# Kernel tuning notes

Hardware: AMD Instinct MI355X
Metric: run time of the kernel (lower is better)

## Reference

```python
import jax, jax.numpy as jnp
import numpy as np

N_HEADS = 16
K_SIZE = 4          # canon conv kernel size
GATE_BIAS = 2.0     # gate_bias_init
GATE_REG = 0.01     # gate_regularization_strength (type='l1')


def setup_inputs() -> dict:
    key = jax.random.key(0)
    ks = jax.random.split(key, 11)
    B, T, C, M = 2, 2048, 1024, 256
    rn = lambda k, shape, s=1.0: jax.random.normal(k, shape, dtype=jnp.float32) * s
    return {
        "x": rn(ks[0], (B, T, C)),
        "forward_memory": rn(ks[1], (B, M, C)),
        "reverse_memory": rn(ks[2], (B, M, C)),
        "w_q": rn(ks[3], (C, C), 0.02),
        "w_k": rn(ks[4], (C, C), 0.02),
        "w_v": rn(ks[5], (C, C), 0.02),
        "w_o": rn(ks[6], (C, C), 0.02),
        "gate_w": rn(ks[7], (C, N_HEADS), 0.02),
        "gate_b": jnp.full((N_HEADS,), GATE_BIAS, dtype=jnp.float32),
        "conv_w": rn(ks[8], (K_SIZE, 1, C), 0.05),  # depthwise, WIO layout
        "conv_b": rn(ks[9], (C,), 0.02),
    }


def reference(x, forward_memory, reverse_memory, w_q, w_k, w_v, w_o,
              gate_w, gate_b, conv_w, conv_b):
    B, T, C = x.shape
    h = N_HEADS
    d = C // h
    # projections; memory K/V use the same k/v projections and concat on seq dim
    q = x @ w_q                                                   # [B,T,C]
    k = jnp.concatenate([x @ w_k, forward_memory @ w_k, reverse_memory @ w_k], axis=1)
    v = jnp.concatenate([x @ w_v, forward_memory @ w_v, reverse_memory @ w_v], axis=1)
    S = k.shape[1]
    qh = q.reshape(B, T, h, d).transpose(0, 2, 1, 3)              # [B,h,T,d]
    kh = k.reshape(B, S, h, d).transpose(0, 2, 1, 3)              # [B,h,S,d]
    vh = v.reshape(B, S, h, d).transpose(0, 2, 1, 3)              # [B,h,S,d]
    scale = 1.0 / np.sqrt(d).astype(np.float32)
    scores = jnp.einsum('bhtd,bhsd->bhts', qh, kh) * scale        # [B,h,T,S]
    # causal mask on the chunk columns only; memory columns always visible
    causal = jnp.triu(jnp.ones((T, T), dtype=bool), 1)
    mask = jnp.concatenate([causal, jnp.zeros((T, S - T), dtype=bool)], axis=1)
    scores = jnp.where(mask[None, None], -jnp.inf, scores)
    w = jax.nn.softmax(scores, axis=-1)
    # split chunk vs memory attention and apply per-head sigmoid gate
    y_chunk = jnp.einsum('bhts,bhsd->bhtd', w[..., :T], vh[:, :, :T])
    y_mem = jnp.einsum('bhts,bhsd->bhtd', w[..., T:], vh[:, :, T:])
    g = jax.nn.sigmoid(q @ gate_w + gate_b)                       # [B,T,h]
    g = g.transpose(0, 2, 1)[..., None]                           # [B,h,T,1]
    y = y_chunk + g * y_mem
    gate_reg_loss = GATE_REG * jnp.mean(jnp.abs(g))
    attn = y.transpose(0, 2, 1, 3).reshape(B, T, C)
    # CanonConv: causal depthwise conv1d with residual
    xp = jnp.pad(attn, ((0, 0), (K_SIZE - 1, 0), (0, 0)))
    conv = jax.lax.conv_general_dilated(
        xp, conv_w, window_strides=(1,), padding='VALID',
        dimension_numbers=('NWC', 'WIO', 'NWC'), feature_group_count=C) + conv_b
    attn = attn + conv
    out = attn @ w_o
    return out, gate_reg_loss
```

## Files before the change

### kernel.cpp

```cpp
#include <hip/hip_runtime.h>
#include <hip/hip_bf16.h>

typedef __attribute__((ext_vector_type(8))) short short8;
typedef __attribute__((ext_vector_type(4))) short short4v;
typedef __attribute__((ext_vector_type(4))) float float4v;

#define B_ 2
#define T_ 2048
#define C_ 1024
#define H_ 16
#define D_ 64
#define M_ 256
#define S_ 2560

static __device__ __forceinline__ float bf2f(short s) {
    union { unsigned int u; float f; } v;
    v.u = ((unsigned int)(unsigned short)s) << 16;
    return v.f;
}
static __device__ __forceinline__ short f2bf(float f) {
    __hip_bfloat16 h = __float2bfloat16(f);
    return *reinterpret_cast<short*>(&h);
}
static __device__ __forceinline__ void gload_lds16(const short* g, short* l) {
    __builtin_amdgcn_global_load_lds(
        (const __attribute__((address_space(1))) void*)g,
        (__attribute__((address_space(3))) void*)l, 16, 0, 0);
}

__global__ __launch_bounds__(256) void cvt_bf16(const float* __restrict__ src,
                                                short* __restrict__ dst, int n8) {
    int i = blockIdx.x * 256 + threadIdx.x;
    if (i >= n8) return;
    float4v a = *(const float4v*)(src + (size_t)i * 8);
    float4v b = *(const float4v*)(src + (size_t)i * 8 + 4);
    short8 o;
    o[0] = f2bf(a[0]); o[1] = f2bf(a[1]); o[2] = f2bf(a[2]); o[3] = f2bf(a[3]);
    o[4] = f2bf(b[0]); o[5] = f2bf(b[1]); o[6] = f2bf(b[2]); o[7] = f2bf(b[3]);
    *(short8*)(dst + (size_t)i * 8) = o;
}

__global__ void transpose_k(const float* __restrict__ W, short* __restrict__ Wt) {
    __shared__ float tile[32][33];
    int tx = threadIdx.x, ty = threadIdx.y;
    int bx = blockIdx.x * 32, by = blockIdx.y * 32;
    tile[ty][tx] = W[(size_t)(by + ty) * 1024 + bx + tx];
    __syncthreads();
    Wt[(size_t)(bx + ty) * 1024 + by + tx] = f2bf(tile[tx][ty]);
}

__global__ __launch_bounds__(256) void gwt_cvt(const float* __restrict__ gw,
                                               short* __restrict__ gwt) {
    int idx = blockIdx.x * 256 + threadIdx.x;
    int h = idx >> 10, k = idx & 1023;
    gwt[idx] = f2bf(8.0f * gw[k * 16 + h]);
}

static __device__ __forceinline__ const short* concat_row(
    const short* x, const short* f, const short* rm, int r) {
    int b = (r >= S_) ? 1 : 0;
    int s = r - b * S_;
    if (s < T_)       return x  + ((size_t)b * T_ + s) * 1024;
    if (s < T_ + M_)  return f  + ((size_t)b * M_ + (s - T_)) * 1024;
    return rm + ((size_t)b * M_ + (s - T_ - M_)) * 1024;
}

__global__ __launch_bounds__(256) void qkv_fused(
    const short* __restrict__ x_bf, const short* __restrict__ fm_bf,
    const short* __restrict__ rm_bf, const short* __restrict__ wq_t,
    const short* __restrict__ wk_t, const short* __restrict__ wv_t,
    short* __restrict__ qb, short* __restrict__ kall,
    short* __restrict__ vallT) {
    __shared__ __align__(16) short As[128 * 32];
    __shared__ __align__(16) short Bs[128 * 32];
    const int tid = threadIdx.x;
    const int bid = blockIdx.x;
    int which, bm, bn;
    if (bid < 256)      { which = 0; bm = bid >> 3; bn = bid & 7; }
    else if (bid < 576) { which = 1; int t = bid - 256; bm = t >> 3; bn = t & 7; }
    else                { which = 2; int t = bid - 576; bm = t >> 3; bn = t & 7; }
    const short* Bt = (which == 0) ? wq_t : (which == 1) ? wk_t : wv_t;

    const int lane = tid & 63, w = tid >> 6;
    const int l15 = lane & 15, quad = lane >> 4;
    const int wm = (w >> 1) * 64, wn = (w & 1) * 64;
    const int sub = lane >> 2, u = lane & 3;

    const short* a0p;
    const short* a1p;
    {
        int r0 = bm * 128 + w * 32 + sub;
        if (which == 0) {
            a0p = x_bf + (size_t)r0 * 1024 + u * 8;
            a1p = x_bf + (size_t)(r0 + 16) * 1024 + u * 8;
        } else {
            a0p = concat_row(x_bf, fm_bf, rm_bf, r0) + u * 8;
            a1p = concat_row(x_bf, fm_bf, rm_bf, r0 + 16) + u * 8;
        }
    }
    const short* b0p = Bt + (size_t)(bn * 128 + w * 32 + sub) * 1024 + u * 8;
    const short* b1p = b0p + (size_t)16 * 1024;
    short* Asw = As + w * 1024;
    short* Bsw = Bs + w * 1024;

    float4v acc[4][4];
    const float4v zero = {0.f, 0.f, 0.f, 0.f};
#pragma unroll
    for (int i = 0; i < 4; ++i)
#pragma unroll
        for (int j = 0; j < 4; ++j) acc[i][j] = zero;

    for (int k0 = 0; k0 < 1024; k0 += 32) {
        __syncthreads();
        gload_lds16(a0p + k0, Asw);
        gload_lds16(a1p + k0, Asw + 512);
        gload_lds16(b0p + k0, Bsw);
        gload_lds16(b1p + k0, Bsw + 512);
        __syncthreads();
        short8 af[4], bfr[4];
#pragma unroll
        for (int i = 0; i < 4; ++i)
            af[i] = *(const short8*)(&As[(wm + i * 16 + l15) * 32 + quad * 8]);
#pragma unroll
        for (int j = 0; j < 4; ++j)
            bfr[j] = *(const short8*)(&Bs[(wn + j * 16 + l15) * 32 + quad * 8]);
#pragma unroll
        for (int i = 0; i < 4; ++i)
#pragma unroll
            for (int j = 0; j < 4; ++j)
                acc[i][j] = __builtin_amdgcn_mfma_f32_16x16x32_bf16(af[i], bfr[j], acc[i][j], 0, 0, 0);
    }

    const int mbase = bm * 128 + wm, nbase = bn * 128 + wn;
    if (which == 2) {
#pragma unroll
        for (int i = 0; i < 4; ++i)
#pragma unroll
            for (int j = 0; j < 4; ++j) {
                int sbase = mbase + i * 16 + quad * 4;
                int ng = nbase + j * 16 + l15;
                int b = (sbase >= S_) ? 1 : 0, s = sbase - b * S_;
                int hh = ng >> 6, d = ng & 63;
                short4v pk;
#pragma unroll
                for (int r = 0; r < 4; ++r) pk[r] = f2bf(acc[i][j][r]);
                *(short4v*)(vallT + ((size_t)((b * 16 + hh) * 64 + d)) * S_ + s) = pk;
            }
    } else {
        short* Co = (which == 0) ? qb : kall;
        const float scale = (which == 0) ? 0.125f : 1.0f;
#pragma unroll
        for (int i = 0; i < 4; ++i)
#pragma unroll
            for (int j = 0; j < 4; ++j)
#pragma unroll
                for (int r = 0; r < 4; ++r) {
                    int mg = mbase + i * 16 + quad * 4 + r;
                    int ng = nbase + j * 16 + l15;
                    Co[(size_t)mg * 1024 + ng] = f2bf(acc[i][j][r] * scale);
                }
    }
}

__global__ __launch_bounds__(256) void gemm128_wo(
    const short* __restrict__ A0, const short* __restrict__ Bt,
    float* __restrict__ Co) {
    __shared__ __align__(16) short As[128 * 32];
    __shared__ __align__(16) short Bs[128 * 32];
    const int tid = threadIdx.x;
    const int bm = blockIdx.y, bn = blockIdx.x;
    const int lane = tid & 63, w = tid >> 6;
    const int l15 = lane & 15, quad = lane >> 4;
    const int wm = (w >> 1) * 64, wn = (w & 1) * 64;
    const int sub = lane >> 2, u = lane & 3;

    const short* a0p = A0 + (size_t)(bm * 128 + w * 32 + sub) * 1024 + u * 8;
    const short* a1p = a0p + (size_t)16 * 1024;
    const short* b0p = Bt + (size_t)(bn * 128 + w * 32 + sub) * 1024 + u * 8;
    const short* b1p = b0p + (size_t)16 * 1024;
    short* Asw = As + w * 1024;
    short* Bsw = Bs + w * 1024;

    float4v acc[4][4];
    const float4v zero = {0.f, 0.f, 0.f, 0.f};
#pragma unroll
    for (int i = 0; i < 4; ++i)
#pragma unroll
        for (int j = 0; j < 4; ++j) acc[i][j] = zero;

    for (int k0 = 0; k0 < 1024; k0 += 32) {
        __syncthreads();
        gload_lds16(a0p + k0, Asw);
        gload_lds16(a1p + k0, Asw + 512);
        gload_lds16(b0p + k0, Bsw);
        gload_lds16(b1p + k0, Bsw + 512);
        __syncthreads();
        short8 af[4], bfr[4];
#pragma unroll
        for (int i = 0; i < 4; ++i)
            af[i] = *(const short8*)(&As[(wm + i * 16 + l15) * 32 + quad * 8]);
#pragma unroll
        for (int j = 0; j < 4; ++j)
            bfr[j] = *(const short8*)(&Bs[(wn + j * 16 + l15) * 32 + quad * 8]);
#pragma unroll
        for (int i = 0; i < 4; ++i)
#pragma unroll
            for (int j = 0; j < 4; ++j)
                acc[i][j] = __builtin_amdgcn_mfma_f32_16x16x32_bf16(af[i], bfr[j], acc[i][j], 0, 0, 0);
    }

    const int mbase = bm * 128 + wm, nbase = bn * 128 + wn;
#pragma unroll
    for (int i = 0; i < 4; ++i)
#pragma unroll
        for (int j = 0; j < 4; ++j)
#pragma unroll
            for (int r = 0; r < 4; ++r)
                Co[(size_t)(mbase + i * 16 + quad * 4 + r) * 1024 + nbase + j * 16 + l15] = acc[i][j][r];
}

__global__ __launch_bounds__(256) void gate_kernel(
    const short* __restrict__ q, const short* __restrict__ gwt,
    const float* __restrict__ gate_b, float* __restrict__ gbuf,
    float* __restrict__ loss) {
    const int tid = threadIdx.x;
    const int lane = tid & 63, w = tid >> 6;
    const int l15 = lane & 15, quad = lane >> 4;
    const int row0 = blockIdx.x * 64 + w * 16;
    const size_t abase = (size_t)(row0 + l15) * 1024;
    const size_t bbase = (size_t)l15 * 1024;

    float4v acc = {0.f, 0.f, 0.f, 0.f};
#pragma unroll 4
    for (int k0 = 0; k0 < 1024; k0 += 32) {
        short8 af = *(const short8*)(q + abase + k0 + quad * 8);
        short8 bf = *(const short8*)(gwt + bbase + k0 + quad * 8);
        acc = __builtin_amdgcn_mfma_f32_16x16x32_bf16(af, bf, acc, 0, 0, 0);
    }
    const int head = l15;
    const int tbase = row0 + quad * 4;
    const int b = tbase >> 11, t = tbase & 2047;
    const float gbias = gate_b[head];
    float4v g;
    float lsum = 0.f;
#pragma unroll
    for (int r = 0; r < 4; ++r) {
        g[r] = 1.0f / (1.0f + __expf(-(acc[r] + gbias)));
        lsum += g[r];
    }
    *(float4v*)(gbuf + ((size_t)(b * 16 + head)) * 2048 + t) = g;
    lsum += __shfl_xor(lsum, 1);  lsum += __shfl_xor(lsum, 2);
    lsum += __shfl_xor(lsum, 4);  lsum += __shfl_xor(lsum, 8);
    lsum += __shfl_xor(lsum, 16); lsum += __shfl_xor(lsum, 32);
    if (lane == 0) atomicAdd(loss, lsum);
}

__global__ __launch_bounds__(256, 3) void attn_kernel(
    const short* __restrict__ q, const short* __restrict__ kall,
    const short* __restrict__ vallT, const float* __restrict__ gbuf,
    short* __restrict__ attn) {
    __shared__ __align__(16) short Kt[64 * 68];
    __shared__ __align__(16) short Vs[64 * 68];
    __shared__ __align__(16) short Pt[4 * 16 * 72];
    const int tid = threadIdx.x;
    const int bid = blockIdx.x;
    const int qt = 31 - (bid >> 5);
    const int bh = bid & 31, b = bh >> 4, h = bh & 15;
    const int q0 = qt * 64;
    const int lane = tid & 63, w = tid >> 6;
    const int l15 = lane & 15, quad = lane >> 4;
    const int srow = tid >> 2, scol = (tid & 3) * 16;

    const int trow = q0 + w * 16 + l15;
    short8 qf[2];
    qf[0] = *(const short8*)(q + ((size_t)(b * T_ + trow)) * 1024 + h * 64 + quad * 8);
    qf[1] = *(const short8*)(q + ((size_t)(b * T_ + trow)) * 1024 + h * 64 + 32 + quad * 8);

    const float4v zero = {0.f, 0.f, 0.f, 0.f};
    float4v acc_c[4], acc_m[4];
#pragma unroll
    for (int n = 0; n < 4; ++n) { acc_c[n] = zero; acc_m[n] = zero; }
    float lsum = 0.0f;

    short* Pw = &Pt[w * 16 * 72];
    const int ntiles = qt + 9;

    const size_t kbase = (size_t)b * S_ * 1024 + h * 64;
    const size_t vbase = (size_t)bh * 64 * S_;

    short8 pk0, pk1, pv0, pv1;
    {
        pk0 = *(const short8*)(kall + kbase + (size_t)srow * 1024 + scol);
        pk1 = *(const short8*)(kall + kbase + (size_t)srow * 1024 + scol + 8);
        pv0 = *(const short8*)(vallT + vbase + (size_t)srow * S_ + scol);
        pv1 = *(const short8*)(vallT + vbase + (size_t)srow * S_ + scol + 8);
    }

    for (int t = 0; t < ntiles; ++t) {
        __syncthreads();
        *(short8*)(&Kt[srow * 68 + scol])     = pk0;
        *(short8*)(&Kt[srow * 68 + scol + 8]) = pk1;
        *(short8*)(&Vs[srow * 68 + scol])     = pv0;
        *(short8*)(&Vs[srow * 68 + scol + 8]) = pv1;
        __syncthreads();
        if (t + 1 < ntiles) {
            const int t1 = t + 1;
            const int s1 = (t1 <= qt) ? t1 * 64 : T_ + (t1 - qt - 1) * 64;
            pk0 = *(const short8*)(kall + kbase + (size_t)(s1 + srow) * 1024 + scol);
            pk1 = *(const short8*)(kall + kbase + (size_t)(s1 + srow) * 1024 + scol + 8);
            pv0 = *(const short8*)(vallT + vbase + (size_t)srow * S_ + s1 + scol);
            pv1 = *(const short8*)(vallT + vbase + (size_t)srow * S_ + s1 + scol + 8);
        }

        float4v c[4];
#pragma unroll
        for (int n = 0; n < 4; ++n) c[n] = zero;
#pragma unroll
        for (int ks = 0; ks < 2; ++ks) {
            short8 kb[4];
#pragma unroll
            for (int n = 0; n < 4; ++n)
                kb[n] = *(const short8*)(&Kt[(n * 16 + l15) * 68 + ks * 32 + quad * 8]);
#pragma unroll
            for (int n = 0; n < 4; ++n)
                c[n] = __builtin_amdgcn_mfma_f32_16x16x32_bf16(kb[n], qf[ks], c[n], 0, 0, 0);
        }

        const bool diag = (t == qt);
#pragma unroll
        for (int n = 0; n < 4; ++n) {
            float p[4];
#pragma unroll
            for (int r = 0; r < 4; ++r) {
                p[r] = __expf(c[n][r] - 8.0f);
                if (diag && (n * 16 + quad * 4 + r > w * 16 + l15)) p[r] = 0.0f;
                lsum += p[r];
            }
            short4v pk4;
#pragma unroll
            for (int r = 0; r < 4; ++r) pk4[r] = f2bf(p[r]);
            *(short4v*)(&Pw[l15 * 72 + n * 16 + quad * 4]) = pk4;
        }

        float4v* accp = (t > qt) ? acc_m : acc_c;
#pragma unroll
        for (int ks = 0; ks < 2; ++ks) {
            short8 pb = *(const short8*)(&Pw[l15 * 72 + ks * 32 + quad * 8]);
#pragma unroll
            for (int m = 0; m < 4; ++m) {
                short8 vb = *(const short8*)(&Vs[(m * 16 + l15) * 68 + ks * 32 + quad * 8]);
                accp[m] = __builtin_amdgcn_mfma_f32_16x16x32_bf16(vb, pb, accp[m], 0, 0, 0);
            }
        }
    }

    lsum += __shfl_xor(lsum, 16);
    lsum += __shfl_xor(lsum, 32);
    const float g = gbuf[((size_t)b * 16 + h) * 2048 + q0 + w * 16 + l15];
    const float inv = 1.0f / lsum;

    __syncthreads();
    short* Dt = Kt;
#pragma unroll
    for (int m = 0; m < 4; ++m) {
        short4v o4;
#pragma unroll
        for (int r = 0; r < 4; ++r)
            o4[r] = f2bf((acc_c[m][r] + g * acc_m[m][r]) * inv);
        *(short4v*)(&Dt[(w * 16 + l15) * 68 + m * 16 + quad * 4]) = o4;
    }
    __syncthreads();
    short8 o0 = *(const short8*)(&Dt[srow * 68 + scol]);
    short8 o1 = *(const short8*)(&Dt[srow * 68 + scol + 8]);
    *(short8*)(attn + ((size_t)(b * T_ + q0 + srow)) * 1024 + h * 64 + scol) = o0;
    *(short8*)(attn + ((size_t)(b * T_ + q0 + srow)) * 1024 + h * 64 + scol + 8) = o1;
}

__global__ __launch_bounds__(256) void conv_kernel(
    const short* __restrict__ attn, const float* __restrict__ conv_w,
    const float* __restrict__ conv_b, short* __restrict__ attn2) {
    const int idx = blockIdx.x * 256 + threadIdx.x;
    const int c8 = (idx & 127) * 8;
    const int bt = idx >> 7;
    const int t = bt & 2047;
    float acc[8];
    short8 base = *(const short8*)(attn + (size_t)bt * 1024 + c8);
#pragma unroll
    for (int jj = 0; jj < 8; ++jj) acc[jj] = bf2f(base[jj]) + conv_b[c8 + jj];
#pragma unroll
    for (int j = 0; j < 4; ++j) {
        int ts = t - 3 + j;
        if (ts >= 0) {
            short8 xv = *(const short8*)(attn + (size_t)(bt - 3 + j) * 1024 + c8);
#pragma unroll
            for (int jj = 0; jj < 8; ++jj)
                acc[jj] += bf2f(xv[jj]) * conv_w[j * 1024 + c8 + jj];
        }
    }
    short8 outv;
#pragma unroll
    for (int jj = 0; jj < 8; ++jj) outv[jj] = f2bf(acc[jj]);
    *(short8*)(attn2 + (size_t)bt * 1024 + c8) = outv;
}

__global__ void loss_fin(const float* __restrict__ loss, float* __restrict__ out) {
    out[0] = 0.01f * loss[0] / 65536.0f;
}

extern "C" void kernel_launch(void* const* d_in, const int* in_sizes, int n_in,
                              void* d_out, int out_size, void* d_ws, size_t ws_size,
                              hipStream_t stream) {
    const float* x  = (const float*)d_in[0];
    const float* fm = (const float*)d_in[1];
    const float* rm = (const float*)d_in[2];
    const float* wq = (const float*)d_in[3];
    const float* wk = (const float*)d_in[4];
    const float* wv = (const float*)d_in[5];
    const float* wo = (const float*)d_in[6];
    const float* gw = (const float*)d_in[7];
    const float* gb = (const float*)d_in[8];
    const float* cw = (const float*)d_in[9];
    const float* cb = (const float*)d_in[10];
    float* out = (float*)d_out;

    char* ws = (char*)d_ws;
    const size_t MB = 1u << 20;
    short* wq_t  = (short*)(ws + 0 * MB);
    short* wk_t  = (short*)(ws + 2 * MB);
    short* wv_t  = (short*)(ws + 4 * MB);
    short* wo_t  = (short*)(ws + 6 * MB);
    short* x_bf  = (short*)(ws + 8 * MB);
    short* fm_bf = (short*)(ws + 16 * MB);
    short* rm_bf = (short*)(ws + 17 * MB);
    short* qb    = (short*)(ws + 18 * MB);
    short* kall  = (short*)(ws + 26 * MB);
    short* vallT = (short*)(ws + 36 * MB);
    float* gbuf  = (float*)(ws + 46 * MB);
    float* lossp = (float*)(ws + 46 * MB + 256 * 1024);
    short* attnb = x_bf;
    short* attn2 = qb;
    short* gwt   = fm_bf;

    cvt_bf16<<<2048, 256, 0, stream>>>(x, x_bf, 524288);
    cvt_bf16<<<256, 256, 0, stream>>>(fm, fm_bf, 65536);
    cvt_bf16<<<256, 256, 0, stream>>>(rm, rm_bf, 65536);

    dim3 tb(32, 32);
    transpose_k<<<dim3(32, 32), tb, 0, stream>>>(wq, wq_t);
    transpose_k<<<dim3(32, 32), tb, 0, stream>>>(wk, wk_t);
    transpose_k<<<dim3(32, 32), tb, 0, stream>>>(wv, wv_t);
    transpose_k<<<dim3(32, 32), tb, 0, stream>>>(wo, wo_t);

    qkv_fused<<<896, 256, 0, stream>>>(x_bf, fm_bf, rm_bf, wq_t, wk_t, wv_t,
                                       qb, kall, vallT);

    hipMemsetAsync(lossp, 0, 4, stream);
    gwt_cvt<<<64, 256, 0, stream>>>(gw, gwt);
    gate_kernel<<<64, 256, 0, stream>>>(qb, gwt, gb, gbuf, lossp);
    attn_kernel<<<1024, 256, 0, stream>>>(qb, kall, vallT, gbuf, attnb);
    conv_kernel<<<2048, 256, 0, stream>>>(attnb, cw, cb, attn2);
    gemm128_wo<<<dim3(8, 32), 256, 0, stream>>>(attn2, wo_t, out);
    loss_fin<<<1, 1, 0, stream>>>(lossp, out + (size_t)4096 * 1024);
}
```

Measured before the change: 272.0 us.

## Fuse prep kernels, fold gate projection into QKV, enlarge attention tiles, retile Wo GEMM

Merges all bf16 conversions, weight transposes and the gate-weight prep into one launch. The gate weight is precomputed as Wq·gate_w, so the gate GEMM runs on x inside the QKV kernel as extra blocks, and the loss finalisation moves into the conv kernel. Attention now processes 128 query rows per block with two query groups per wave, which halves K/V tile loads per query but lowers occupancy. The Wo GEMM uses 64x128 tiles to launch more blocks. Together these cut launch count and memory traffic, at the cost of more register pressure and a gate precomputation that runs in fp32 on the device.

```diff
diff --git a/kernel.cpp b/kernel.cpp
--- a/kernel.cpp
+++ b/kernel.cpp
@@ -28,32 +28,53 @@
         (__attribute__((address_space(3))) void*)l, 16, 0, 0);
 }
 
-__global__ __launch_bounds__(256) void cvt_bf16(const float* __restrict__ src,
-                                                short* __restrict__ dst, int n8) {
-    int i = blockIdx.x * 256 + threadIdx.x;
-    if (i >= n8) return;
-    float4v a = *(const float4v*)(src + (size_t)i * 8);
-    float4v b = *(const float4v*)(src + (size_t)i * 8 + 4);
-    short8 o;
-    o[0] = f2bf(a[0]); o[1] = f2bf(a[1]); o[2] = f2bf(a[2]); o[3] = f2bf(a[3]);
-    o[4] = f2bf(b[0]); o[5] = f2bf(b[1]); o[6] = f2bf(b[2]); o[7] = f2bf(b[3]);
-    *(short8*)(dst + (size_t)i * 8) = o;
-}
-
-__global__ void transpose_k(const float* __restrict__ W, short* __restrict__ Wt) {
+__global__ __launch_bounds__(256) void prep_kernel(
+    const float* __restrict__ x, const float* __restrict__ fm,
+    const float* __restrict__ rm, const float* __restrict__ wq,
+    const float* __restrict__ wk, const float* __restrict__ wv,
+    const float* __restrict__ wo, const float* __restrict__ gw,
+    short* __restrict__ x_bf, short* __restrict__ fm_bf,
+    short* __restrict__ rm_bf, short* __restrict__ wq_t,
+    short* __restrict__ wk_t, short* __restrict__ wv_t,
+    short* __restrict__ wo_t, short* __restrict__ wg2t,
+    float* __restrict__ lossp) {
     __shared__ float tile[32][33];
-    int tx = threadIdx.x, ty = threadIdx.y;
-    int bx = blockIdx.x * 32, by = blockIdx.y * 32;
-    tile[ty][tx] = W[(size_t)(by + ty) * 1024 + bx + tx];
-    __syncthreads();
-    Wt[(size_t)(bx + ty) * 1024 + by + tx] = f2bf(tile[tx][ty]);
-}
-
-__global__ __launch_bounds__(256) void gwt_cvt(const float* __restrict__ gw,
-                                               short* __restrict__ gwt) {
-    int idx = blockIdx.x * 256 + threadIdx.x;
-    int h = idx >> 10, k = idx & 1023;
-    gwt[idx] = f2bf(8.0f * gw[k * 16 + h]);
+    const int bid = blockIdx.x, tid = threadIdx.x;
+    if (bid < 2560) {
+        const float* src; short* dst; int i;
+        if (bid < 2048)      { src = x;  dst = x_bf;  i = bid * 256 + tid; }
+        else if (bid < 2304) { src = fm; dst = fm_bf; i = (bid - 2048) * 256 + tid; }
+        else                 { src = rm; dst = rm_bf; i = (bid - 2304) * 256 + tid; }
+        float4v a = *(const float4v*)(src + (size_t)i * 8);
+        float4v b = *(const float4v*)(src + (size_t)i * 8 + 4);
+        short8 o;
+        o[0] = f2bf(a[0]); o[1] = f2bf(a[1]); o[2] = f2bf(a[2]); o[3] = f2bf(a[3]);
+        o[4] = f2bf(b[0]); o[5] = f2bf(b[1]); o[6] = f2bf(b[2]); o[7] = f2bf(b[3]);
+        *(short8*)(dst + (size_t)i * 8) = o;
+    } else if (bid < 6656) {
+        const int g = bid - 2560;
+        const int m = g >> 10, tI = g & 1023;
+        const float* W = (m == 0) ? wq : (m == 1) ? wk : (m == 2) ? wv : wo;
+        short* Wt      = (m == 0) ? wq_t : (m == 1) ? wk_t : (m == 2) ? wv_t : wo_t;
+        const int ty = tid >> 5, tx = tid & 31;
+        const int bx = (tI & 31) << 5, by = (tI >> 5) << 5;
+#pragma unroll
+        for (int r = 0; r < 4; ++r)
+            tile[ty + r * 8][tx] = W[(size_t)(by + ty + r * 8) * 1024 + bx + tx];
+        __syncthreads();
+#pragma unroll
+        for (int r = 0; r < 4; ++r)
+            Wt[(size_t)(bx + ty + r * 8) * 1024 + by + tx] = f2bf(tile[tx][ty + r * 8]);
+    } else {
+        if (bid == 6656 && tid == 0) *lossp = 0.0f;
+        const int idx = (bid - 6656) * 256 + tid;
+        const int k = idx >> 4, hh = idx & 15;
+        float acc = 0.0f;
+#pragma unroll 4
+        for (int c = 0; c < 1024; ++c)
+            acc += wq[(size_t)k * 1024 + c] * gw[c * 16 + hh];
+        wg2t[hh * 1024 + k] = f2bf(acc);
+    }
 }
 
 static __device__ __forceinline__ const short* concat_row(
@@ -69,20 +90,54 @@
     const short* __restrict__ x_bf, const short* __restrict__ fm_bf,
     const short* __restrict__ rm_bf, const short* __restrict__ wq_t,
     const short* __restrict__ wk_t, const short* __restrict__ wv_t,
+    const short* __restrict__ wg2t, const float* __restrict__ gate_b,
     short* __restrict__ qb, short* __restrict__ kall,
-    short* __restrict__ vallT) {
+    short* __restrict__ vallT, float* __restrict__ gbuf,
+    float* __restrict__ loss) {
     __shared__ __align__(16) short As[128 * 32];
     __shared__ __align__(16) short Bs[128 * 32];
     const int tid = threadIdx.x;
     const int bid = blockIdx.x;
+    const int lane = tid & 63, w = tid >> 6;
+    const int l15 = lane & 15, quad = lane >> 4;
+
+    if (bid >= 896) {
+        const int gblk = bid - 896;
+        const int row0 = gblk * 64 + w * 16;
+        const size_t abase = (size_t)(row0 + l15) * 1024;
+        const size_t bbase = (size_t)l15 * 1024;
+        float4v acc = {0.f, 0.f, 0.f, 0.f};
+#pragma unroll 4
+        for (int k0 = 0; k0 < 1024; k0 += 32) {
+            short8 af = *(const short8*)(x_bf + abase + k0 + quad * 8);
+            short8 bf = *(const short8*)(wg2t + bbase + k0 + quad * 8);
+            acc = __builtin_amdgcn_mfma_f32_16x16x32_bf16(af, bf, acc, 0, 0, 0);
+        }
+        const int head = l15;
+        const int tbase = row0 + quad * 4;
+        const int b = tbase >> 11, t = tbase & 2047;
+        const float gbias = gate_b[head];
+        float4v g;
+        float lsum = 0.f;
+#pragma unroll
+        for (int r = 0; r < 4; ++r) {
+            g[r] = 1.0f / (1.0f + __expf(-(acc[r] + gbias)));
+            lsum += g[r];
+        }
+        *(float4v*)(gbuf + ((size_t)(b * 16 + head)) * 2048 + t) = g;
+        lsum += __shfl_xor(lsum, 1);  lsum += __shfl_xor(lsum, 2);
+        lsum += __shfl_xor(lsum, 4);  lsum += __shfl_xor(lsum, 8);
+        lsum += __shfl_xor(lsum, 16); lsum += __shfl_xor(lsum, 32);
+        if (lane == 0) atomicAdd(loss, lsum);
+        return;
+    }
+
     int which, bm, bn;
     if (bid < 256)      { which = 0; bm = bid >> 3; bn = bid & 7; }
     else if (bid < 576) { which = 1; int t = bid - 256; bm = t >> 3; bn = t & 7; }
     else                { which = 2; int t = bid - 576; bm = t >> 3; bn = t & 7; }
     const short* Bt = (which == 0) ? wq_t : (which == 1) ? wk_t : wv_t;
 
-    const int lane = tid & 63, w = tid >> 6;
-    const int l15 = lane & 15, quad = lane >> 4;
     const int wm = (w >> 1) * 64, wn = (w & 1) * 64;
     const int sub = lane >> 2, u = lane & 3;
 
@@ -162,249 +217,231 @@
     }
 }
 
-__global__ __launch_bounds__(256) void gemm128_wo(
+__global__ __launch_bounds__(256, 2) void attn_kernel(
+    const short* __restrict__ q, const short* __restrict__ kall,
+    const short* __restrict__ vallT, const float* __restrict__ gbuf,
+    short* __restrict__ attn) {
+    __shared__ __align__(16) short KV[128 * 68];
+    __shared__ __align__(16) short Pt[4 * 32 * 68];
+    const int tid = threadIdx.x;
+    const int bid = blockIdx.x;
+    const int qt = 15 - (bid >> 5);
+    const int bh = bid & 31, b = bh >> 4, h = bh & 15;
+    const int q0 = qt * 128;
+    const int lane = tid & 63, w = tid >> 6;
+    const int l15 = lane & 15, quad = lane >> 4;
+    const int srow = tid >> 2, scol = (tid & 3) * 16;
+    short* Kt = KV;
+    short* Vs = KV + 64 * 68;
+
+    short8 qf[2][2];
+#pragma unroll
+    for (int qg = 0; qg < 2; ++qg)
+#pragma unroll
+        for (int ks = 0; ks < 2; ++ks)
+            qf[qg][ks] = *(const short8*)(q + ((size_t)(b * T_ + q0 + w * 32 + qg * 16 + l15)) * 1024
+                                          + h * 64 + ks * 32 + quad * 8);
+
+    const float4v zero = {0.f, 0.f, 0.f, 0.f};
+    float4v accC[2][4], accM[2][4];
+#pragma unroll
+    for (int g = 0; g < 2; ++g)
+#pragma unroll
+        for (int m = 0; m < 4; ++m) { accC[g][m] = zero; accM[g][m] = zero; }
+    float lsum[2] = {0.0f, 0.0f};
+
+    short* Pw = &Pt[w * 32 * 68];
+    const int ntiles = 2 * qt + 10;
+
+    const size_t kbase = (size_t)b * S_ * 1024 + h * 64;
+    const size_t vbase = (size_t)bh * 64 * S_;
+
+    short8 pk0, pk1, pv0, pv1;
+    pk0 = *(const short8*)(kall + kbase + (size_t)srow * 1024 + scol);
+    pk1 = *(const short8*)(kall + kbase + (size_t)srow * 1024 + scol + 8);
+    pv0 = *(const short8*)(vallT + vbase + (size_t)srow * S_ + scol);
+    pv1 = *(const short8*)(vallT + vbase + (size_t)srow * S_ + scol + 8);
+
+    for (int t = 0; t < ntiles; ++t) {
+        __syncthreads();
+        *(short8*)(&Kt[srow * 68 + scol])     = pk0;
+        *(short8*)(&Kt[srow * 68 + scol + 8]) = pk1;
+        *(short8*)(&Vs[srow * 68 + scol])     = pv0;
+        *(short8*)(&Vs[srow * 68 + scol + 8]) = pv1;
+        __syncthreads();
+        if (t + 1 < ntiles) {
+            const int t1 = t + 1;
+            const int s1 = (t1 <= 2 * qt + 1) ? t1 * 64 : T_ + (t1 - 2 * qt - 2) * 64;
+            pk0 = *(const short8*)(kall + kbase + (size_t)(s1 + srow) * 1024 + scol);
+            pk1 = *(const short8*)(kall + kbase + (size_t)(s1 + srow) * 1024 + scol + 8);
+            pv0 = *(const short8*)(vallT + vbase + (size_t)srow * S_ + s1 + scol);
+            pv1 = *(const short8*)(vallT + vbase + (size_t)srow * S_ + s1 + scol + 8);
+        }
+
+        short8 kb[2][4], vb[2][4];
+#pragma unroll
+        for (int ks = 0; ks < 2; ++ks)
+#pragma unroll
+            for (int n = 0; n < 4; ++n) {
+                kb[ks][n] = *(const short8*)(&Kt[(n * 16 + l15) * 68 + ks * 32 + quad * 8]);
+                vb[ks][n] = *(const short8*)(&Vs[(n * 16 + l15) * 68 + ks * 32 + quad * 8]);
+            }
+
+        const bool last2 = (t >= 2 * qt) && (t <= 2 * qt + 1);
+        const bool mem = (t > 2 * qt + 1);
+        const int srel = (t - 2 * qt) * 64;
+
+#pragma unroll
+        for (int qg = 0; qg < 2; ++qg) {
+            const int qmin = w * 32 + qg * 16;
+            if (last2 && srel > qmin + 15) continue;
+
+            float4v c[4];
+#pragma unroll
+            for (int n = 0; n < 4; ++n) c[n] = zero;
+#pragma unroll
+            for (int ks = 0; ks < 2; ++ks)
+#pragma unroll
+                for (int n = 0; n < 4; ++n)
+                    c[n] = __builtin_amdgcn_mfma_f32_16x16x32_bf16(kb[ks][n], qf[qg][ks], c[n], 0, 0, 0);
+
+#pragma unroll
+            for (int n = 0; n < 4; ++n) {
+                float p[4];
+                short4v pk4;
+#pragma unroll
+                for (int r = 0; r < 4; ++r) {
+                    p[r] = __expf(c[n][r] - 8.0f);
+                    if (last2 && (srel + n * 16 + quad * 4 + r > qmin + l15)) p[r] = 0.0f;
+                    lsum[qg] += p[r];
+                    pk4[r] = f2bf(p[r]);
+                }
+                *(short4v*)(&Pw[(qg * 16 + l15) * 68 + n * 16 + quad * 4]) = pk4;
+            }
+
+            float4v* accp = mem ? accM[qg] : accC[qg];
+#pragma unroll
+            for (int ks = 0; ks < 2; ++ks) {
+                short8 pb = *(const short8*)(&Pw[(qg * 16 + l15) * 68 + ks * 32 + quad * 8]);
+#pragma unroll
+                for (int m = 0; m < 4; ++m)
+                    accp[m] = __builtin_amdgcn_mfma_f32_16x16x32_bf16(vb[ks][m], pb, accp[m], 0, 0, 0);
+            }
+        }
+    }
+
+    __syncthreads();
+    short* Dt = KV;
+#pragma unroll
+    for (int qg = 0; qg < 2; ++qg) {
+        float ls = lsum[qg];
+        ls += __shfl_xor(ls, 16);
+        ls += __shfl_xor(ls, 32);
+        const int ql = w * 32 + qg * 16 + l15;
+        const float g = gbuf[((size_t)b * 16 + h) * 2048 + q0 + ql];
+        const float inv = 1.0f / ls;
+#pragma unroll
+        for (int m = 0; m < 4; ++m) {
+            short4v o4;
+#pragma unroll
+            for (int r = 0; r < 4; ++r)
+                o4[r] = f2bf((accC[qg][m][r] + g * accM[qg][m][r]) * inv);
+            *(short4v*)(&Dt[ql * 68 + m * 16 + quad * 4]) = o4;
+        }
+    }
+    __syncthreads();
+    const int orow = tid >> 1, ocol = (tid & 1) * 32;
+    const size_t obase = ((size_t)(b * T_ + q0 + orow)) * 1024 + h * 64 + ocol;
+#pragma unroll
+    for (int u2 = 0; u2 < 4; ++u2) {
+        short8 ov = *(const short8*)(&Dt[orow * 68 + ocol + u2 * 8]);
+        *(short8*)(attn + obase + u2 * 8) = ov;
+    }
+}
+
+__global__ __launch_bounds__(256) void conv_kernel(
+    const short* __restrict__ attn, const float* __restrict__ conv_w,
+    const float* __restrict__ conv_b, short* __restrict__ attn2,
+    const float* __restrict__ lossp, float* __restrict__ out) {
+    const int idx = blockIdx.x * 256 + threadIdx.x;
+    if (idx == 0) out[(size_t)4096 * 1024] = 0.01f * lossp[0] / 65536.0f;
+    const int c8 = (idx & 127) * 8;
+    const int bt = idx >> 7;
+    const int t = bt & 2047;
+    float acc[8];
+    short8 base = *(const short8*)(attn + (size_t)bt * 1024 + c8);
+#pragma unroll
+    for (int jj = 0; jj < 8; ++jj) acc[jj] = bf2f(base[jj]) + conv_b[c8 + jj];
+#pragma unroll
+    for (int j = 0; j < 4; ++j) {
+        int ts = t - 3 + j;
+        if (ts >= 0) {
+            short8 xv = *(const short8*)(attn + (size_t)(bt - 3 + j) * 1024 + c8);
+#pragma unroll
+            for (int jj = 0; jj < 8; ++jj)
+                acc[jj] += bf2f(xv[jj]) * conv_w[j * 1024 + c8 + jj];
+        }
+    }
+    short8 outv;
+#pragma unroll
+    for (int jj = 0; jj < 8; ++jj) outv[jj] = f2bf(acc[jj]);
+    *(short8*)(attn2 + (size_t)bt * 1024 + c8) = outv;
+}
+
+__global__ __launch_bounds__(256) void wo_gemm(
     const short* __restrict__ A0, const short* __restrict__ Bt,
     float* __restrict__ Co) {
-    __shared__ __align__(16) short As[128 * 32];
+    __shared__ __align__(16) short As[64 * 32];
     __shared__ __align__(16) short Bs[128 * 32];
     const int tid = threadIdx.x;
     const int bm = blockIdx.y, bn = blockIdx.x;
     const int lane = tid & 63, w = tid >> 6;
     const int l15 = lane & 15, quad = lane >> 4;
-    const int wm = (w >> 1) * 64, wn = (w & 1) * 64;
-    const int sub = lane >> 2, u = lane & 3;
-
-    const short* a0p = A0 + (size_t)(bm * 128 + w * 32 + sub) * 1024 + u * 8;
-    const short* a1p = a0p + (size_t)16 * 1024;
-    const short* b0p = Bt + (size_t)(bn * 128 + w * 32 + sub) * 1024 + u * 8;
-    const short* b1p = b0p + (size_t)16 * 1024;
-    short* Asw = As + w * 1024;
-    short* Bsw = Bs + w * 1024;
-
-    float4v acc[4][4];
+    const int wm = (w >> 1) * 32, wn = (w & 1) * 64;
+    const int sr = lane >> 2, u = lane & 3;
+
+    const short* ap  = A0 + (size_t)(bm * 64 + w * 16 + sr) * 1024 + u * 8;
+    const short* b0p = Bt + (size_t)(bn * 128 + w * 16 + sr) * 1024 + u * 8;
+    const short* b1p = b0p + (size_t)64 * 1024;
+    short* Asw  = As + w * 512;
+    short* Bsw0 = Bs + w * 512;
+    short* Bsw1 = Bs + 2048 + w * 512;
+
+    float4v acc[2][4];
     const float4v zero = {0.f, 0.f, 0.f, 0.f};
 #pragma unroll
-    for (int i = 0; i < 4; ++i)
+    for (int i = 0; i < 2; ++i)
 #pragma unroll
         for (int j = 0; j < 4; ++j) acc[i][j] = zero;
 
     for (int k0 = 0; k0 < 1024; k0 += 32) {
         __syncthreads();
-        gload_lds16(a0p + k0, Asw);
-        gload_lds16(a1p + k0, Asw + 512);
-        gload_lds16(b0p + k0, Bsw);
-        gload_lds16(b1p + k0, Bsw + 512);
-        __syncthreads();
-        short8 af[4], bfr[4];
-#pragma unroll
-        for (int i = 0; i < 4; ++i)
+        gload_lds16(ap + k0, Asw);
+        gload_lds16(b0p + k0, Bsw0);
+        gload_lds16(b1p + k0, Bsw1);
+        __syncthreads();
+        short8 af[2], bfr[4];
+#pragma unroll
+        for (int i = 0; i < 2; ++i)
             af[i] = *(const short8*)(&As[(wm + i * 16 + l15) * 32 + quad * 8]);
 #pragma unroll
         for (int j = 0; j < 4; ++j)
             bfr[j] = *(const short8*)(&Bs[(wn + j * 16 + l15) * 32 + quad * 8]);
 #pragma unroll
-        for (int i = 0; i < 4; ++i)
+        for (int i = 0; i < 2; ++i)
 #pragma unroll
             for (int j = 0; j < 4; ++j)
                 acc[i][j] = __builtin_amdgcn_mfma_f32_16x16x32_bf16(af[i], bfr[j], acc[i][j], 0, 0, 0);
     }
 
-    const int mbase = bm * 128 + wm, nbase = bn * 128 + wn;
-#pragma unroll
-    for (int i = 0; i < 4; ++i)
+    const int mbase = bm * 64 + wm, nbase = bn * 128 + wn;
+#pragma unroll
+    for (int i = 0; i < 2; ++i)
 #pragma unroll
         for (int j = 0; j < 4; ++j)
 #pragma unroll
             for (int r = 0; r < 4; ++r)
                 Co[(size_t)(mbase + i * 16 + quad * 4 + r) * 1024 + nbase + j * 16 + l15] = acc[i][j][r];
-}
-
-__global__ __launch_bounds__(256) void gate_kernel(
-    const short* __restrict__ q, const short* __restrict__ gwt,
-    const float* __restrict__ gate_b, float* __restrict__ gbuf,
-    float* __restrict__ loss) {
-    const int tid = threadIdx.x;
-    const int lane = tid & 63, w = tid >> 6;
-    const int l15 = lane & 15, quad = lane >> 4;
-    const int row0 = blockIdx.x * 64 + w * 16;
-    const size_t abase = (size_t)(row0 + l15) * 1024;
-    const size_t bbase = (size_t)l15 * 1024;
-
-    float4v acc = {0.f, 0.f, 0.f, 0.f};
-#pragma unroll 4
-    for (int k0 = 0; k0 < 1024; k0 += 32) {
-        short8 af = *(const short8*)(q + abase + k0 + quad * 8);
-        short8 bf = *(const short8*)(gwt + bbase + k0 + quad * 8);
-        acc = __builtin_amdgcn_mfma_f32_16x16x32_bf16(af, bf, acc, 0, 0, 0);
-    }
-    const int head = l15;
-    const int tbase = row0 + quad * 4;
-    const int b = tbase >> 11, t = tbase & 2047;
-    const float gbias = gate_b[head];
-    float4v g;
-    float lsum = 0.f;
-#pragma unroll
-    for (int r = 0; r < 4; ++r) {
-        g[r] = 1.0f / (1.0f + __expf(-(acc[r] + gbias)));
-        lsum += g[r];
-    }
-    *(float4v*)(gbuf + ((size_t)(b * 16 + head)) * 2048 + t) = g;
-    lsum += __shfl_xor(lsum, 1);  lsum += __shfl_xor(lsum, 2);
-    lsum += __shfl_xor(lsum, 4);  lsum += __shfl_xor(lsum, 8);
-    lsum += __shfl_xor(lsum, 16); lsum += __shfl_xor(lsum, 32);
-    if (lane == 0) atomicAdd(loss, lsum);
-}
-
-__global__ __launch_bounds__(256, 3) void attn_kernel(
-    const short* __restrict__ q, const short* __restrict__ kall,
-    const short* __restrict__ vallT, const float* __restrict__ gbuf,
-    short* __restrict__ attn) {
-    __shared__ __align__(16) short Kt[64 * 68];
-    __shared__ __align__(16) short Vs[64 * 68];
-    __shared__ __align__(16) short Pt[4 * 16 * 72];
-    const int tid = threadIdx.x;
-    const int bid = blockIdx.x;
-    const int qt = 31 - (bid >> 5);
-    const int bh = bid & 31, b = bh >> 4, h = bh & 15;
-    const int q0 = qt * 64;
-    const int lane = tid & 63, w = tid >> 6;
-    const int l15 = lane & 15, quad = lane >> 4;
-    const int srow = tid >> 2, scol = (tid & 3) * 16;
-
-    const int trow = q0 + w * 16 + l15;
-    short8 qf[2];
-    qf[0] = *(const short8*)(q + ((size_t)(b * T_ + trow)) * 1024 + h * 64 + quad * 8);
-    qf[1] = *(const short8*)(q + ((size_t)(b * T_ + trow)) * 1024 + h * 64 + 32 + quad * 8);
-
-    const float4v zero = {0.f, 0.f, 0.f, 0.f};
-    float4v acc_c[4], acc_m[4];
-#pragma unroll
-    for (int n = 0; n < 4; ++n) { acc_c[n] = zero; acc_m[n] = zero; }
-    float lsum = 0.0f;
-
-    short* Pw = &Pt[w * 16 * 72];
-    const int ntiles = qt + 9;
-
-    const size_t kbase = (size_t)b * S_ * 1024 + h * 64;
-    const size_t vbase = (size_t)bh * 64 * S_;
-
-    short8 pk0, pk1, pv0, pv1;
-    {
-        pk0 = *(const short8*)(kall + kbase + (size_t)srow * 1024 + scol);
-        pk1 = *(const short8*)(kall + kbase + (size_t)srow * 1024 + scol + 8);
-        pv0 = *(const short8*)(vallT + vbase + (size_t)srow * S_ + scol);
-        pv1 = *(const short8*)(vallT + vbase + (size_t)srow * S_ + scol + 8);
-    }
-
-    for (int t = 0; t < ntiles; ++t) {
-        __syncthreads();
-        *(short8*)(&Kt[srow * 68 + scol])     = pk0;
-        *(short8*)(&Kt[srow * 68 + scol + 8]) = pk1;
-        *(short8*)(&Vs[srow * 68 + scol])     = pv0;
-        *(short8*)(&Vs[srow * 68 + scol + 8]) = pv1;
-        __syncthreads();
-        if (t + 1 < ntiles) {
-            const int t1 = t + 1;
-            const int s1 = (t1 <= qt) ? t1 * 64 : T_ + (t1 - qt - 1) * 64;
-            pk0 = *(const short8*)(kall + kbase + (size_t)(s1 + srow) * 1024 + scol);
-            pk1 = *(const short8*)(kall + kbase + (size_t)(s1 + srow) * 1024 + scol + 8);
-            pv0 = *(const short8*)(vallT + vbase + (size_t)srow * S_ + s1 + scol);
-            pv1 = *(const short8*)(vallT + vbase + (size_t)srow * S_ + s1 + scol + 8);
-        }
-
-        float4v c[4];
-#pragma unroll
-        for (int n = 0; n < 4; ++n) c[n] = zero;
-#pragma unroll
-        for (int ks = 0; ks < 2; ++ks) {
-            short8 kb[4];
-#pragma unroll
-            for (int n = 0; n < 4; ++n)
-                kb[n] = *(const short8*)(&Kt[(n * 16 + l15) * 68 + ks * 32 + quad * 8]);
-#pragma unroll
-            for (int n = 0; n < 4; ++n)
-                c[n] = __builtin_amdgcn_mfma_f32_16x16x32_bf16(kb[n], qf[ks], c[n], 0, 0, 0);
-        }
-
-        const bool diag = (t == qt);
-#pragma unroll
-        for (int n = 0; n < 4; ++n) {
-            float p[4];
-#pragma unroll
-            for (int r = 0; r < 4; ++r) {
-                p[r] = __expf(c[n][r] - 8.0f);
-                if (diag && (n * 16 + quad * 4 + r > w * 16 + l15)) p[r] = 0.0f;
-                lsum += p[r];
-            }
-            short4v pk4;
-#pragma unroll
-            for (int r = 0; r < 4; ++r) pk4[r] = f2bf(p[r]);
-            *(short4v*)(&Pw[l15 * 72 + n * 16 + quad * 4]) = pk4;
-        }
-
-        float4v* accp = (t > qt) ? acc_m : acc_c;
-#pragma unroll
-        for (int ks = 0; ks < 2; ++ks) {
-            short8 pb = *(const short8*)(&Pw[l15 * 72 + ks * 32 + quad * 8]);
-#pragma unroll
-            for (int m = 0; m < 4; ++m) {
-                short8 vb = *(const short8*)(&Vs[(m * 16 + l15) * 68 + ks * 32 + quad * 8]);
-                accp[m] = __builtin_amdgcn_mfma_f32_16x16x32_bf16(vb, pb, accp[m], 0, 0, 0);
-            }
-        }
-    }
-
-    lsum += __shfl_xor(lsum, 16);
-    lsum += __shfl_xor(lsum, 32);
-    const float g = gbuf[((size_t)b * 16 + h) * 2048 + q0 + w * 16 + l15];
-    const float inv = 1.0f / lsum;
-
-    __syncthreads();
-    short* Dt = Kt;
-#pragma unroll
-    for (int m = 0; m < 4; ++m) {
-        short4v o4;
-#pragma unroll
-        for (int r = 0; r < 4; ++r)
-            o4[r] = f2bf((acc_c[m][r] + g * acc_m[m][r]) * inv);
-        *(short4v*)(&Dt[(w * 16 + l15) * 68 + m * 16 + quad * 4]) = o4;
-    }
-    __syncthreads();
-    short8 o0 = *(const short8*)(&Dt[srow * 68 + scol]);
-    short8 o1 = *(const short8*)(&Dt[srow * 68 + scol + 8]);
-    *(short8*)(attn + ((size_t)(b * T_ + q0 + srow)) * 1024 + h * 64 + scol) = o0;
-    *(short8*)(attn + ((size_t)(b * T_ + q0 + srow)) * 1024 + h * 64 + scol + 8) = o1;
-}
-
-__global__ __launch_bounds__(256) void conv_kernel(
-    const short* __restrict__ attn, const float* __restrict__ conv_w,
-    const float* __restrict__ conv_b, short* __restrict__ attn2) {
-    const int idx = blockIdx.x * 256 + threadIdx.x;
-    const int c8 = (idx & 127) * 8;
-    const int bt = idx >> 7;
-    const int t = bt & 2047;
-    float acc[8];
-    short8 base = *(const short8*)(attn + (size_t)bt * 1024 + c8);
-#pragma unroll
-    for (int jj = 0; jj < 8; ++jj) acc[jj] = bf2f(base[jj]) + conv_b[c8 + jj];
-#pragma unroll
-    for (int j = 0; j < 4; ++j) {
-        int ts = t - 3 + j;
-        if (ts >= 0) {
-            short8 xv = *(const short8*)(attn + (size_t)(bt - 3 + j) * 1024 + c8);
-#pragma unroll
-            for (int jj = 0; jj < 8; ++jj)
-                acc[jj] += bf2f(xv[jj]) * conv_w[j * 1024 + c8 + jj];
-        }
-    }
-    short8 outv;
-#pragma unroll
-    for (int jj = 0; jj < 8; ++jj) outv[jj] = f2bf(acc[jj]);
-    *(short8*)(attn2 + (size_t)bt * 1024 + c8) = outv;
-}
-
-__global__ void loss_fin(const float* __restrict__ loss, float* __restrict__ out) {
-    out[0] = 0.01f * loss[0] / 65536.0f;
 }
 
 extern "C" void kernel_launch(void* const* d_in, const int* in_sizes, int n_in,
@@ -436,29 +473,17 @@
     short* kall  = (short*)(ws + 26 * MB);
     short* vallT = (short*)(ws + 36 * MB);
     float* gbuf  = (float*)(ws + 46 * MB);
-    float* lossp = (float*)(ws + 46 * MB + 256 * 1024);
+    float* lossp = (float*)(ws + 46 * MB + 262144);
+    short* wg2t  = (short*)(ws + 46 * MB + 262144 + 256);
     short* attnb = x_bf;
     short* attn2 = qb;
-    short* gwt   = fm_bf;
-
-    cvt_bf16<<<2048, 256, 0, stream>>>(x, x_bf, 524288);
-    cvt_bf16<<<256, 256, 0, stream>>>(fm, fm_bf, 65536);
-    cvt_bf16<<<256, 256, 0, stream>>>(rm, rm_bf, 65536);
-
-    dim3 tb(32, 32);
-    transpose_k<<<dim3(32, 32), tb, 0, stream>>>(wq, wq_t);
-    transpose_k<<<dim3(32, 32), tb, 0, stream>>>(wk, wk_t);
-    transpose_k<<<dim3(32, 32), tb, 0, stream>>>(wv, wv_t);
-    transpose_k<<<dim3(32, 32), tb, 0, stream>>>(wo, wo_t);
-
-    qkv_fused<<<896, 256, 0, stream>>>(x_bf, fm_bf, rm_bf, wq_t, wk_t, wv_t,
-                                       qb, kall, vallT);
-
-    hipMemsetAsync(lossp, 0, 4, stream);
-    gwt_cvt<<<64, 256, 0, stream>>>(gw, gwt);
-    gate_kernel<<<64, 256, 0, stream>>>(qb, gwt, gb, gbuf, lossp);
-    attn_kernel<<<1024, 256, 0, stream>>>(qb, kall, vallT, gbuf, attnb);
-    conv_kernel<<<2048, 256, 0, stream>>>(attnb, cw, cb, attn2);
-    gemm128_wo<<<dim3(8, 32), 256, 0, stream>>>(attn2, wo_t, out);
-    loss_fin<<<1, 1, 0, stream>>>(lossp, out + (size_t)4096 * 1024);
-}
+
+    prep_kernel<<<6720, 256, 0, stream>>>(x, fm, rm, wq, wk, wv, wo, gw,
+                                          x_bf, fm_bf, rm_bf, wq_t, wk_t, wv_t,
+                                          wo_t, wg2t, lossp);
+    qkv_fused<<<960, 256, 0, stream>>>(x_bf, fm_bf, rm_bf, wq_t, wk_t, wv_t,
+                                       wg2t, gb, qb, kall, vallT, gbuf, lossp);
+    attn_kernel<<<512, 256, 0, stream>>>(qb, kall, vallT, gbuf, attnb);
+    conv_kernel<<<2048, 256, 0, stream>>>(attnb, cw, cb, attn2, lossp, out);
+    wo_gemm<<<dim3(8, 64), 256, 0, stream>>>(attn2, wo_t, out);
+}
```

After: 428.6 us. +57.6%, slower.
